# Kernel tuning notes

Measured on AMD Instinct MI355X. Metric: run time of the kernel, lower is better.

The kernel has to match this reference:

```python
import jax, jax.numpy as jnp
import numpy as np

IDF, CDF = 128, 256
B, IH, IW, SL = 16, 128, 128, 48

def setup_inputs() -> dict:
    key = jax.random.key(0)
    ks = jax.random.split(key, 8)
    mask = jax.random.randint(ks[3], (B, SL), 0, 2).astype(bool)
    mask = mask.at[:, 0].set(False)  # ensure at least one unmasked word per row
    return {
        "input": jax.random.normal(ks[0], (B, IDF, IH, IW), jnp.float32),
        "sentence": jax.random.normal(ks[1], (B, 100), jnp.float32),
        "context": jax.random.normal(ks[2], (B, CDF, SL), jnp.float32),
        "mask": mask,
        "w_ctx": jax.random.normal(ks[4], (IDF, CDF), jnp.float32) * 0.05,
        "w_sv": jax.random.normal(ks[5], (IDF, IDF), jnp.float32) * 0.05,
        "w_lin": jax.random.normal(ks[6], (IDF, 100), jnp.float32) * 0.05,
        "b_lin": jax.random.normal(ks[7], (IDF,), jnp.float32) * 0.05,
    }

def reference(input, sentence, context, mask, w_ctx, w_sv, w_lin, b_lin):
    b, idf, ih, iw = input.shape
    q = ih * iw
    sl = context.shape[2]
    target = input.reshape(b, idf, q)                       # b,idf,q
    sourceT = jnp.einsum('ic,bcs->bis', w_ctx, context)     # conv1x1 on context
    attn = jnp.einsum('biq,bis->bqs', target, sourceT)      # b,q,s
    attn = jnp.where(mask[:, None, :], -jnp.inf, attn)      # masked_fill
    attn = jax.nn.softmax(attn, axis=-1)                    # softmax over sourceL
    weightedContext = jnp.einsum('bis,bqs->biq', sourceT, attn).reshape(b, idf, ih, iw)
    word_attn = jnp.swapaxes(attn, 1, 2).reshape(b, sl, ih, iw)
    sent = sentence @ w_lin.T + b_lin                       # b,idf
    sent = sent[:, :, None, None]                           # b,idf,1,1 (broadcast)
    sentence_vs = input * sent
    sentence_vs = jnp.einsum('oi,bihw->bohw', w_sv, sentence_vs)  # conv1x1
    sent_att = jax.nn.softmax(sentence_vs, axis=1)          # nn.Softmax() on 4D -> dim=1
    weightedSentence = sent * sent_att                      # broadcast of repeated sentence
    return (weightedContext, weightedSentence, word_attn, sent_att)
```

## Files before the change

### kernel.cpp

```cpp
#include <hip/hip_runtime.h>
#include <math.h>
#include <stdint.h>

#define BB  16
#define IDF 128
#define CDF 256
#define SL  48
#define QQ  16384
#define QT  64

typedef short bf16x8 __attribute__((ext_vector_type(8)));
typedef short bf16x4 __attribute__((ext_vector_type(4)));
typedef float f32x4  __attribute__((ext_vector_type(4)));

__device__ __forceinline__ short f2bf(float f) {
    uint32_t u = __builtin_bit_cast(uint32_t, f);
    u += 0x7FFFu + ((u >> 16) & 1u);
    return (short)(u >> 16);
}
__device__ __forceinline__ float bf2f(short h) {
    uint32_t u = ((uint32_t)(unsigned short)h) << 16;
    return __builtin_bit_cast(float, u);
}

__global__ __launch_bounds__(256) void prepM_kernel(
    const float* __restrict__ context,
    const float* __restrict__ w_ctx,
    const float* __restrict__ sentence,
    const float* __restrict__ w_lin,
    const float* __restrict__ b_lin,
    const float* __restrict__ w_sv,
    float* __restrict__ sentW,
    short* __restrict__ wsvS,
    short* __restrict__ stB,
    short* __restrict__ stC)
{
    const int b = blockIdx.x;
    const int t = threadIdx.x;
    const int wv = t >> 6, l = t & 63;
    const int c = l & 15, g = l >> 4;

    __shared__ __align__(16) short ctxT_h[SL * CDF];
    __shared__ __align__(16) short ctxT_l[SL * CDF];
    __shared__ float srcTile[IDF * SL];
    __shared__ float sent_sh[IDF];

    if (t < IDF) {
        float a = b_lin[t];
        for (int k = 0; k < 100; ++k)
            a += sentence[b * 100 + k] * w_lin[t * 100 + k];
        sent_sh[t] = a;
        sentW[b * IDF + t] = a;
    }

    for (int r = 0; r < 6; ++r) {
        int task = r * 256 + t;
        int cp = task & 127, s4 = task >> 7;
        int cd = cp * 2, sb = s4 * 4;
        const float* row0 = context + ((size_t)b * CDF + cd) * SL + sb;
        const float4 va = *(const float4*)(row0);
        const float4 vb = *(const float4*)(row0 + SL);
        float va_[4] = {va.x, va.y, va.z, va.w};
        float vb_[4] = {vb.x, vb.y, vb.z, vb.w};
        #pragma unroll
        for (int j = 0; j < 4; ++j) {
            int s = sb + j;
            short h0 = f2bf(va_[j]), h1 = f2bf(vb_[j]);
            short l0 = f2bf(va_[j] - bf2f(h0)), l1 = f2bf(vb_[j] - bf2f(h1));
            int e = s * CDF + (cd ^ ((s & 15) << 3));
            *(uint32_t*)(ctxT_h + e) = (uint32_t)(uint16_t)h0 | ((uint32_t)(uint16_t)h1 << 16);
            *(uint32_t*)(ctxT_l + e) = (uint32_t)(uint16_t)l0 | ((uint32_t)(uint16_t)l1 << 16);
        }
    }
    __syncthreads();

    #pragma unroll
    for (int mi = 0; mi < 2; ++mi) {
        const int Mt = wv * 2 + mi;
        const int m = 16 * Mt + c;
        bf16x8 Ah[8], Al[8];
        #pragma unroll
        for (int ks = 0; ks < 8; ++ks) {
            const float* wp = w_ctx + m * CDF + 8 * g + 32 * ks;
            const float4 f0 = *(const float4*)(wp);
            const float4 f1 = *(const float4*)(wp + 4);
            float fv[8] = {f0.x, f0.y, f0.z, f0.w, f1.x, f1.y, f1.z, f1.w};
            #pragma unroll
            for (int j = 0; j < 8; ++j) {
                short h = f2bf(fv[j]);
                Ah[ks][j] = h;
                Al[ks][j] = f2bf(fv[j] - bf2f(h));
            }
        }
        #pragma unroll
        for (int Nt = 0; Nt < 3; ++Nt) {
            const int s = 16 * Nt + c;
            f32x4 acc = {0.f, 0.f, 0.f, 0.f};
            #pragma unroll
            for (int ks = 0; ks < 8; ++ks) {
                int e = s * CDF + ((8 * g + 32 * ks) ^ ((s & 15) << 3));
                const bf16x8 Bh = *(const bf16x8*)(ctxT_h + e);
                const bf16x8 Bl = *(const bf16x8*)(ctxT_l + e);
                acc = __builtin_amdgcn_mfma_f32_16x16x32_bf16(Ah[ks], Bh, acc, 0, 0, 0);
                acc = __builtin_amdgcn_mfma_f32_16x16x32_bf16(Ah[ks], Bl, acc, 0, 0, 0);
                acc = __builtin_amdgcn_mfma_f32_16x16x32_bf16(Al[ks], Bh, acc, 0, 0, 0);
            }
            #pragma unroll
            for (int r = 0; r < 4; ++r)
                srcTile[(16 * Mt + 4 * g + r) * SL + s] = acc[r];
        }
    }
    __syncthreads();

    #pragma unroll
    for (int cc = 0; cc < 3; ++cc) {
        int comb = wv * 3 + cc;
        int Mt = comb >> 2, ks = comb & 3;
        int s = c + 16 * Mt;
        int ib = 8 * g + 32 * ks;
        bf16x8 hv, lv;
        #pragma unroll
        for (int j = 0; j < 8; ++j) {
            float v = srcTile[(ib + j) * SL + s];
            short h = f2bf(v);
            hv[j] = h;
            lv[j] = f2bf(v - bf2f(h));
        }
        size_t base = (size_t)b * 12288 + (((Mt * 4 + ks) * 2) * 64 + l) * 8;
        *(bf16x8*)(stB + base) = hv;
        *(bf16x8*)(stB + base + 512) = lv;
    }
    #pragma unroll
    for (int cc = 0; cc < 4; ++cc) {
        int comb = wv * 4 + cc;
        int Mt = comb >> 1, ks = comb & 1;
        int i = c + 16 * Mt;
        int sb = 8 * g + 32 * ks;
        bf16x8 v8;
        #pragma unroll
        for (int j = 0; j < 8; ++j) {
            int s = sb + j;
            v8[j] = (s < SL) ? f2bf(srcTile[i * SL + s]) : (short)0;
        }
        *(bf16x8*)(stC + (size_t)b * 8192 + ((Mt * 2 + ks) * 64 + l) * 8) = v8;
    }
    #pragma unroll
    for (int cc = 0; cc < 8; ++cc) {
        int comb = wv * 8 + cc;
        int Mt = comb >> 2, ks = comb & 3;
        int o = c + 16 * Mt;
        int ib = g * 8 + 32 * ks;
        bf16x8 outv;
        #pragma unroll
        for (int j = 0; j < 8; ++j)
            outv[j] = f2bf(w_sv[o * IDF + ib + j] * sent_sh[ib + j]);
        *(bf16x8*)(wsvS + (size_t)b * 16384 + ((Mt * 4 + ks) * 64 + l) * 8) = outv;
    }
}

__global__ __launch_bounds__(256, 4) void fused_kernel(
    const float* __restrict__ input,
    const short* __restrict__ stB,
    const short* __restrict__ stC,
    const short* __restrict__ wsvS,
    const float* __restrict__ sentW,
    const int*   __restrict__ mask,
    float* __restrict__ wctx, float* __restrict__ wsent,
    float* __restrict__ wattn, float* __restrict__ satt)
{
    const int bid = blockIdx.x;
    const int b   = bid >> 8;
    const int q0  = (bid & 255) * QT;
    const int t   = threadIdx.x;
    const int w   = t >> 6;
    const int l   = t & 63;
    const int c   = l & 15;
    const int g   = l >> 4;

    __shared__ __align__(16) short xq[2 * QT * IDF];
    __shared__ float sbias[SL];
    __shared__ float sent_lds[IDF];

    short* xqh = xq;
    short* xql = xq + QT * IDF;

    {
        const int qb = (t & 15) * 4;
        #pragma unroll
        for (int r = 0; r < 4; ++r) {
            int i = (r * 16 + (t >> 4)) * 2;
            const float4 va = *(const float4*)(input + ((size_t)b * IDF + i    ) * QQ + q0 + qb);
            const float4 vb = *(const float4*)(input + ((size_t)b * IDF + i + 1) * QQ + q0 + qb);
            float va_[4] = {va.x, va.y, va.z, va.w};
            float vb_[4] = {vb.x, vb.y, vb.z, vb.w};
            #pragma unroll
            for (int jj = 0; jj < 4; ++jj) {
                int q = qb + jj;
                short h0 = f2bf(va_[jj]);
                short h1 = f2bf(vb_[jj]);
                short l0 = f2bf(va_[jj] - bf2f(h0));
                short l1 = f2bf(vb_[jj] - bf2f(h1));
                int e = q * IDF + (i ^ ((q & 15) << 3));
                *(uint32_t*)(xqh + e) = (uint32_t)(uint16_t)h0 | ((uint32_t)(uint16_t)h1 << 16);
                *(uint32_t*)(xql + e) = (uint32_t)(uint16_t)l0 | ((uint32_t)(uint16_t)l1 << 16);
            }
        }
    }
    if (t < SL)  sbias[t] = mask[b * SL + t] ? -INFINITY : 0.f;
    if (t < IDF) sent_lds[t] = sentW[b * IDF + t];
    __syncthreads();

    const int qrow = 16 * w + c;
    const short* xh_p = xqh + qrow * IDF;
    const short* xl_p = xql + qrow * IDF;
    bf16x8 fxh[4], fxl[4];
    #pragma unroll
    for (int ks = 0; ks < 4; ++ks) {
        int off = (32 * ks + 8 * g) ^ (c << 3);
        fxh[ks] = *(const bf16x8*)(xh_p + off);
        fxl[ks] = *(const bf16x8*)(xl_p + off);
    }
    __syncthreads();

    short* attq = xql;
    {
        bf16x8 z = {0, 0, 0, 0, 0, 0, 0, 0};
        *(bf16x8*)(attq + w * 1024 + l * 16) = z;
        *(bf16x8*)(attq + w * 1024 + l * 16 + 8) = z;
    }

    const int q = q0 + qrow;

    const short* stBb = stB + (size_t)b * 12288;
    f32x4 accB[3];
    #pragma unroll
    for (int Mt = 0; Mt < 3; ++Mt) {
        f32x4 a = {0.f, 0.f, 0.f, 0.f};
        #pragma unroll
        for (int ks = 0; ks < 4; ++ks) {
            const bf16x8 sh = *(const bf16x8*)(stBb + ((((Mt * 4 + ks) * 2 + 0) * 64 + l) * 8));
            const bf16x8 sl = *(const bf16x8*)(stBb + ((((Mt * 4 + ks) * 2 + 1) * 64 + l) * 8));
            a = __builtin_amdgcn_mfma_f32_16x16x32_bf16(sh, fxh[ks], a, 0, 0, 0);
            a = __builtin_amdgcn_mfma_f32_16x16x32_bf16(sh, fxl[ks], a, 0, 0, 0);
            a = __builtin_amdgcn_mfma_f32_16x16x32_bf16(sl, fxh[ks], a, 0, 0, 0);
        }
        accB[Mt] = a;
    }

    float mx = -INFINITY;
    #pragma unroll
    for (int Mt = 0; Mt < 3; ++Mt)
        #pragma unroll
        for (int r = 0; r < 4; ++r) {
            int s = 16 * Mt + 4 * g + r;
            float lv = accB[Mt][r] + sbias[s];
            accB[Mt][r] = lv;
            mx = fmaxf(mx, lv);
        }
    mx = fmaxf(mx, __shfl_xor(mx, 16));
    mx = fmaxf(mx, __shfl_xor(mx, 32));
    float sum = 0.f;
    #pragma unroll
    for (int Mt = 0; Mt < 3; ++Mt)
        #pragma unroll
        for (int r = 0; r < 4; ++r) {
            float e = __expf(accB[Mt][r] - mx);
            accB[Mt][r] = e;
            sum += e;
        }
    sum += __shfl_xor(sum, 16);
    sum += __shfl_xor(sum, 32);
    float inv = 1.f / sum;
    #pragma unroll
    for (int Mt = 0; Mt < 3; ++Mt) {
        bf16x4 pv;
        #pragma unroll
        for (int r = 0; r < 4; ++r) {
            int s = 16 * Mt + 4 * g + r;
            float p = accB[Mt][r] * inv;
            __builtin_nontemporal_store(p, wattn + ((size_t)b * SL + s) * QQ + q);
            pv[r] = f2bf(p);
        }
        int sbase = 16 * Mt + 4 * g;
        *(bf16x4*)(attq + w * 1024 + c * 64 + (sbase ^ ((c & 7) << 3))) = pv;
    }

    bf16x8 fat[2];
    #pragma unroll
    for (int ks = 0; ks < 2; ++ks)
        fat[ks] = *(const bf16x8*)(attq + w * 1024 + c * 64 +
                                   ((32 * ks + 8 * g) ^ ((c & 7) << 3)));

    const short* wsb = wsvS + (size_t)b * 16384;
    f32x4 accA[8];
    #pragma unroll
    for (int Mt = 0; Mt < 8; ++Mt) accA[Mt] = (f32x4){0.f, 0.f, 0.f, 0.f};
    #pragma unroll
    for (int Mt = 0; Mt < 8; ++Mt) {
        #pragma unroll
        for (int ks = 0; ks < 4; ++ks) {
            const bf16x8 wf = *(const bf16x8*)(wsb + (((Mt * 4 + ks) * 64 + l) * 8));
            accA[Mt] = __builtin_amdgcn_mfma_f32_16x16x32_bf16(wf, fxh[ks], accA[Mt], 0, 0, 0);
        }
    }
    float mA = -INFINITY;
    #pragma unroll
    for (int Mt = 0; Mt < 8; ++Mt)
        #pragma unroll
        for (int r = 0; r < 4; ++r) mA = fmaxf(mA, accA[Mt][r]);
    mA = fmaxf(mA, __shfl_xor(mA, 16));
    mA = fmaxf(mA, __shfl_xor(mA, 32));
    float sA = 0.f;
    #pragma unroll
    for (int Mt = 0; Mt < 8; ++Mt)
        #pragma unroll
        for (int r = 0; r < 4; ++r) {
            float e = __expf(accA[Mt][r] - mA);
            accA[Mt][r] = e;
            sA += e;
        }
    sA += __shfl_xor(sA, 16);
    sA += __shfl_xor(sA, 32);
    float invA = 1.f / sA;

    float* tile = (float*)xq;
    __syncthreads();

    #pragma unroll
    for (int Mt = 0; Mt < 8; ++Mt)
        #pragma unroll
        for (int r = 0; r < 4; ++r)
            tile[(16 * Mt + 4 * g + r) * 64 + qrow] = accA[Mt][r] * invA;
    __syncthreads();

    #pragma unroll
    for (int k = 0; k < 8; ++k) {
        int idx = k * 256 + t;
        int o = idx >> 4, q4 = idx & 15;
        f32x4 v = ((const f32x4*)tile)[idx];
        size_t base = ((size_t)b * IDF + o) * QQ + q0 + q4 * 4;
        __builtin_nontemporal_store(v, (f32x4*)(satt + base));
        float sc = sent_lds[o];
        f32x4 vs = v * sc;
        __builtin_nontemporal_store(vs, (f32x4*)(wsent + base));
    }

    const short* stCb = stC + (size_t)b * 8192;
    f32x4 accC[8];
    #pragma unroll
    for (int Mt = 0; Mt < 8; ++Mt) {
        f32x4 a = {0.f, 0.f, 0.f, 0.f};
        #pragma unroll
        for (int ks = 0; ks < 2; ++ks) {
            const bf16x8 cf = *(const bf16x8*)(stCb + (((Mt * 2 + ks) * 64 + l) * 8));
            a = __builtin_amdgcn_mfma_f32_16x16x32_bf16(cf, fat[ks], a, 0, 0, 0);
        }
        accC[Mt] = a;
    }
    __syncthreads();

    #pragma unroll
    for (int Mt = 0; Mt < 8; ++Mt)
        #pragma unroll
        for (int r = 0; r < 4; ++r)
            tile[(16 * Mt + 4 * g + r) * 64 + qrow] = accC[Mt][r];
    __syncthreads();

    #pragma unroll
    for (int k = 0; k < 8; ++k) {
        int idx = k * 256 + t;
        int o = idx >> 4, q4 = idx & 15;
        f32x4 v = ((const f32x4*)tile)[idx];
        size_t base = ((size_t)b * IDF + o) * QQ + q0 + q4 * 4;
        __builtin_nontemporal_store(v, (f32x4*)(wctx + base));
    }
}

extern "C" void kernel_launch(void* const* d_in, const int* in_sizes, int n_in,
                              void* d_out, int out_size, void* d_ws, size_t ws_size,
                              hipStream_t stream) {
    const float* input    = (const float*)d_in[0];
    const float* sentence = (const float*)d_in[1];
    const float* context  = (const float*)d_in[2];
    const int*   mask     = (const int*)d_in[3];
    const float* w_ctx    = (const float*)d_in[4];
    const float* w_sv     = (const float*)d_in[5];
    const float* w_lin    = (const float*)d_in[6];
    const float* b_lin    = (const float*)d_in[7];

    float* out = (float*)d_out;
    float* out_wctx  = out;
    float* out_wsent = out + (size_t)BB * IDF * QQ;
    float* out_wattn = out + 2 * (size_t)BB * IDF * QQ;
    float* out_satt  = out_wattn + (size_t)BB * SL * QQ;

    float* ws    = (float*)d_ws;
    float* sentW = ws;
    short* wsvS  = (short*)(ws + 2048);
    short* stB   = wsvS + 262144;
    short* stC   = stB + 196608;

    prepM_kernel<<<dim3(16), 256, 0, stream>>>(context, w_ctx, sentence,
                                               w_lin, b_lin, w_sv,
                                               sentW, wsvS, stB, stC);
    fused_kernel<<<dim3(4096), 256, 0, stream>>>(input, stB, stC, wsvS, sentW,
                                                 mask, out_wctx, out_wsent,
                                                 out_wattn, out_satt);
}
```

Baseline: 136.6 us.

## Stage word-attention stores through swizzled LDS and precompute mask bias

Word-attention probabilities were written as scattered scalar nontemporal stores. They now go through an LDS tile and are written back as coalesced float4 rows. The LDS transpose tiles get an XOR swizzle to cut bank conflicts, and the mask bias moves into the prep kernel so the main kernel needs less LDS, which supports a raised occupancy hint (5 blocks per CU). The residual bf16 split now truncates instead of rounding, to save ALU work. This adds extra syncthreads and may push register pressure under the tighter launch bound.

```diff
diff --git a/kernel.cpp b/kernel.cpp
--- a/kernel.cpp
+++ b/kernel.cpp
@@ -17,6 +17,9 @@
     uint32_t u = __builtin_bit_cast(uint32_t, f);
     u += 0x7FFFu + ((u >> 16) & 1u);
     return (short)(u >> 16);
+}
+__device__ __forceinline__ short f2bf_t(float f) {
+    return (short)(__builtin_bit_cast(uint32_t, f) >> 16);
 }
 __device__ __forceinline__ float bf2f(short h) {
     uint32_t u = ((uint32_t)(unsigned short)h) << 16;
@@ -30,7 +33,9 @@
     const float* __restrict__ w_lin,
     const float* __restrict__ b_lin,
     const float* __restrict__ w_sv,
+    const int*   __restrict__ mask,
     float* __restrict__ sentW,
+    float* __restrict__ biasB,
     short* __restrict__ wsvS,
     short* __restrict__ stB,
     short* __restrict__ stC)
@@ -51,6 +56,10 @@
             a += sentence[b * 100 + k] * w_lin[t * 100 + k];
         sent_sh[t] = a;
         sentW[b * IDF + t] = a;
+    }
+    if (t >= IDF && t < IDF + SL) {
+        int s = t - IDF;
+        biasB[b * SL + s] = mask[b * SL + s] ? -INFINITY : 0.f;
     }
 
     for (int r = 0; r < 6; ++r) {
@@ -66,7 +75,7 @@
         for (int j = 0; j < 4; ++j) {
             int s = sb + j;
             short h0 = f2bf(va_[j]), h1 = f2bf(vb_[j]);
-            short l0 = f2bf(va_[j] - bf2f(h0)), l1 = f2bf(vb_[j] - bf2f(h1));
+            short l0 = f2bf_t(va_[j] - bf2f(h0)), l1 = f2bf_t(vb_[j] - bf2f(h1));
             int e = s * CDF + (cd ^ ((s & 15) << 3));
             *(uint32_t*)(ctxT_h + e) = (uint32_t)(uint16_t)h0 | ((uint32_t)(uint16_t)h1 << 16);
             *(uint32_t*)(ctxT_l + e) = (uint32_t)(uint16_t)l0 | ((uint32_t)(uint16_t)l1 << 16);
@@ -89,7 +98,7 @@
             for (int j = 0; j < 8; ++j) {
                 short h = f2bf(fv[j]);
                 Ah[ks][j] = h;
-                Al[ks][j] = f2bf(fv[j] - bf2f(h));
+                Al[ks][j] = f2bf_t(fv[j] - bf2f(h));
             }
         }
         #pragma unroll
@@ -124,7 +133,7 @@
             float v = srcTile[(ib + j) * SL + s];
             short h = f2bf(v);
             hv[j] = h;
-            lv[j] = f2bf(v - bf2f(h));
+            lv[j] = f2bf_t(v - bf2f(h));
         }
         size_t base = (size_t)b * 12288 + (((Mt * 4 + ks) * 2) * 64 + l) * 8;
         *(bf16x8*)(stB + base) = hv;
@@ -158,13 +167,13 @@
     }
 }
 
-__global__ __launch_bounds__(256, 4) void fused_kernel(
+__global__ __launch_bounds__(256, 5) void fused_kernel(
     const float* __restrict__ input,
     const short* __restrict__ stB,
     const short* __restrict__ stC,
     const short* __restrict__ wsvS,
     const float* __restrict__ sentW,
-    const int*   __restrict__ mask,
+    const float* __restrict__ biasB,
     float* __restrict__ wctx, float* __restrict__ wsent,
     float* __restrict__ wattn, float* __restrict__ satt)
 {
@@ -178,8 +187,6 @@
     const int g   = l >> 4;
 
     __shared__ __align__(16) short xq[2 * QT * IDF];
-    __shared__ float sbias[SL];
-    __shared__ float sent_lds[IDF];
 
     short* xqh = xq;
     short* xql = xq + QT * IDF;
@@ -198,16 +205,14 @@
                 int q = qb + jj;
                 short h0 = f2bf(va_[jj]);
                 short h1 = f2bf(vb_[jj]);
-                short l0 = f2bf(va_[jj] - bf2f(h0));
-                short l1 = f2bf(vb_[jj] - bf2f(h1));
+                short l0 = f2bf_t(va_[jj] - bf2f(h0));
+                short l1 = f2bf_t(vb_[jj] - bf2f(h1));
                 int e = q * IDF + (i ^ ((q & 15) << 3));
                 *(uint32_t*)(xqh + e) = (uint32_t)(uint16_t)h0 | ((uint32_t)(uint16_t)h1 << 16);
                 *(uint32_t*)(xql + e) = (uint32_t)(uint16_t)l0 | ((uint32_t)(uint16_t)l1 << 16);
             }
         }
     }
-    if (t < SL)  sbias[t] = mask[b * SL + t] ? -INFINITY : 0.f;
-    if (t < IDF) sent_lds[t] = sentW[b * IDF + t];
     __syncthreads();
 
     const int qrow = 16 * w + c;
@@ -223,6 +228,7 @@
     __syncthreads();
 
     short* attq = xql;
+    float* wtile = (float*)xqh;
     {
         bf16x8 z = {0, 0, 0, 0, 0, 0, 0, 0};
         *(bf16x8*)(attq + w * 1024 + l * 16) = z;
@@ -249,14 +255,15 @@
 
     float mx = -INFINITY;
     #pragma unroll
-    for (int Mt = 0; Mt < 3; ++Mt)
-        #pragma unroll
-        for (int r = 0; r < 4; ++r) {
-            int s = 16 * Mt + 4 * g + r;
-            float lv = accB[Mt][r] + sbias[s];
+    for (int Mt = 0; Mt < 3; ++Mt) {
+        const f32x4 bias4 = *(const f32x4*)(biasB + b * SL + 16 * Mt + 4 * g);
+        #pragma unroll
+        for (int r = 0; r < 4; ++r) {
+            float lv = accB[Mt][r] + bias4[r];
             accB[Mt][r] = lv;
             mx = fmaxf(mx, lv);
         }
+    }
     mx = fmaxf(mx, __shfl_xor(mx, 16));
     mx = fmaxf(mx, __shfl_xor(mx, 32));
     float sum = 0.f;
@@ -278,7 +285,7 @@
         for (int r = 0; r < 4; ++r) {
             int s = 16 * Mt + 4 * g + r;
             float p = accB[Mt][r] * inv;
-            __builtin_nontemporal_store(p, wattn + ((size_t)b * SL + s) * QQ + q);
+            wtile[s * 64 + (qrow ^ (((s >> 2) & 3) << 4))] = p;
             pv[r] = f2bf(p);
         }
         int sbase = 16 * Mt + 4 * g;
@@ -323,25 +330,35 @@
     sA += __shfl_xor(sA, 32);
     float invA = 1.f / sA;
 
+    __syncthreads();
+
+    #pragma unroll
+    for (int k = 0; k < 3; ++k) {
+        int idx = k * 256 + t;
+        int s = idx >> 4, q4 = idx & 15;
+        f32x4 v = ((const f32x4*)wtile)[s * 16 + (q4 ^ (((s >> 2) & 3) << 2))];
+        __builtin_nontemporal_store(v, (f32x4*)(wattn + ((size_t)b * SL + s) * QQ + q0 + q4 * 4));
+    }
+    __syncthreads();
+
     float* tile = (float*)xq;
-    __syncthreads();
-
     #pragma unroll
     for (int Mt = 0; Mt < 8; ++Mt)
         #pragma unroll
-        for (int r = 0; r < 4; ++r)
-            tile[(16 * Mt + 4 * g + r) * 64 + qrow] = accA[Mt][r] * invA;
+        for (int r = 0; r < 4; ++r) {
+            int o = 16 * Mt + 4 * g + r;
+            tile[o * 64 + (qrow ^ (((o >> 2) & 3) << 4))] = accA[Mt][r] * invA;
+        }
     __syncthreads();
 
     #pragma unroll
     for (int k = 0; k < 8; ++k) {
         int idx = k * 256 + t;
         int o = idx >> 4, q4 = idx & 15;
-        f32x4 v = ((const f32x4*)tile)[idx];
+        f32x4 v = ((const f32x4*)tile)[o * 16 + (q4 ^ (((o >> 2) & 3) << 2))];
         size_t base = ((size_t)b * IDF + o) * QQ + q0 + q4 * 4;
         __builtin_nontemporal_store(v, (f32x4*)(satt + base));
-        float sc = sent_lds[o];
-        f32x4 vs = v * sc;
+        f32x4 vs = v * sentW[b * IDF + o];
         __builtin_nontemporal_store(vs, (f32x4*)(wsent + base));
     }
 
@@ -362,17 +379,18 @@
     #pragma unroll
     for (int Mt = 0; Mt < 8; ++Mt)
         #pragma unroll
-        for (int r = 0; r < 4; ++r)
-            tile[(16 * Mt + 4 * g + r) * 64 + qrow] = accC[Mt][r];
+        for (int r = 0; r < 4; ++r) {
+            int o = 16 * Mt + 4 * g + r;
+            tile[o * 64 + (qrow ^ (((o >> 2) & 3) << 4))] = accC[Mt][r];
+        }
     __syncthreads();
 
     #pragma unroll
     for (int k = 0; k < 8; ++k) {
         int idx = k * 256 + t;
         int o = idx >> 4, q4 = idx & 15;
-        f32x4 v = ((const f32x4*)tile)[idx];
-        size_t base = ((size_t)b * IDF + o) * QQ + q0 + q4 * 4;
-        __builtin_nontemporal_store(v, (f32x4*)(wctx + base));
+        f32x4 v = ((const f32x4*)tile)[o * 16 + (q4 ^ (((o >> 2) & 3) << 2))];
+        __builtin_nontemporal_store(v, (f32x4*)(wctx + ((size_t)b * IDF + o) * QQ + q0 + q4 * 4));
     }
 }
 
@@ -396,14 +414,16 @@
 
     float* ws    = (float*)d_ws;
     float* sentW = ws;
-    short* wsvS  = (short*)(ws + 2048);
+    float* biasB = ws + 2048;
+    short* wsvS  = (short*)(ws + 2816);
     short* stB   = wsvS + 262144;
     short* stC   = stB + 196608;
 
     prepM_kernel<<<dim3(16), 256, 0, stream>>>(context, w_ctx, sentence,
-                                               w_lin, b_lin, w_sv,
-                                               sentW, wsvS, stB, stC);
-    fused_kernel<<<dim3(4096), 256, 0, stream>>>(input, stB, stC, wsvS, sentW,
-                                                 mask, out_wctx, out_wsent,
+                                               w_lin, b_lin, w_sv, mask,
+                                               sentW, biasB, wsvS, stB, stC);
+    fused_kernel<<<dim3(4096), 256, 0, stream>>>(input, stB, stC, wsvS,
+                                                 sentW, biasB,
+                                                 out_wctx, out_wsent,
                                                  out_wattn, out_satt);
 }
```

After: 147.2 us. 1.08x slower.
